# Kernel optimization log

Hardware: AMD Instinct MI355X
Metric: run time of the kernel (lower is better)

## Reference

```python
import jax, jax.numpy as jnp
import numpy as np

B, T, F, U = 256, 512, 128, 1024  # batch, seq_len, feature dim, lstm units


def setup_inputs() -> dict:
    key = jax.random.key(0)
    ks = jax.random.split(key, 11)
    s = jnp.float32(0.05)  # small init so tanh/sigmoid stay in useful range
    f32 = jnp.float32
    return {
        "input_tensor": jax.random.normal(ks[0], (B, T, F), f32),
        # encoder LSTM weights (keras gate order i,f,c,o packed along last axis)
        "enc_Wx": jax.random.normal(ks[1], (F, 4 * U), f32) * s,
        "enc_Wh": jax.random.normal(ks[2], (U, 4 * U), f32) * s,
        "enc_b": jax.random.normal(ks[3], (4 * U,), f32) * s,
        # decoder LSTMCell weights (input dim = U, since it is fed its own output)
        "dec_Wx": jax.random.normal(ks[4], (U, 4 * U), f32) * s,
        "dec_Wh": jax.random.normal(ks[5], (U, 4 * U), f32) * s,
        "dec_b": jax.random.normal(ks[6], (4 * U,), f32) * s,
        # dense1: U -> U with relu; dense2: U -> F linear
        "d1_W": jax.random.normal(ks[7], (U, U), f32) * s,
        "d1_b": jax.random.normal(ks[8], (U,), f32) * s,
        "d2_W": jax.random.normal(ks[9], (U, F), f32) * s,
        "d2_b": jax.random.normal(ks[10], (F,), f32) * s,
    }


def _lstm_step(Wx, Wh, b):
    """Standard keras LSTM cell step. Gate packing order: i, f, g(cand), o."""
    def step(carry, x_t):
        h, c = carry
        z = x_t @ Wx + h @ Wh + b  # [B, 4U]
        i, f, g, o = jnp.split(z, 4, axis=-1)
        c = jax.nn.sigmoid(f) * c + jax.nn.sigmoid(i) * jnp.tanh(g)
        h = jax.nn.sigmoid(o) * jnp.tanh(c)
        return (h, c), h
    return step


def reference(input_tensor, enc_Wx, enc_Wh, enc_b, dec_Wx, dec_Wh, dec_b,
              d1_W, d1_b, d2_W, d2_b):
    x = input_tensor
    b_sz, t_len = x.shape[0], x.shape[1]
    u = enc_Wh.shape[0]
    h0 = jnp.zeros((b_sz, u), x.dtype)

    # Encoder: run LSTM over time, keep only final (h, c) (return_state=True).
    (h, c), _ = jax.lax.scan(_lstm_step(enc_Wx, enc_Wh, enc_b), (h0, h0),
                             jnp.swapaxes(x, 0, 1))  # xs: [T, B, F]

    # Decoder: feed previous output back as input, T steps.
    dec_step = _lstm_step(dec_Wx, dec_Wh, dec_b)
    def dec(carry, _):
        x_in, hh, cc = carry
        (hh, cc), _ = dec_step((hh, cc), x_in)
        return (hh, hh, cc), hh  # next input is the new hidden output

    _, hs = jax.lax.scan(dec, (h, h, c), None, length=t_len)  # hs: [T, B, U]

    # Per-step projections, fused over all timesteps (same math as in-loop dense).
    y = jnp.maximum(hs @ d1_W + d1_b, 0.0) @ d2_W + d2_b  # [T, B, F]
    return jnp.swapaxes(y, 0, 1)  # [B, T, F]
```

## Files before the change

kernel.cpp:

```cpp
#include <hip/hip_runtime.h>
#include <hip/hip_bf16.h>
#include <math.h>
#include <stdio.h>


typedef __attribute__((ext_vector_type(8))) short short8;
typedef __attribute__((ext_vector_type(4))) float f32x4;

#define MFMA(a, b, c) __builtin_amdgcn_mfma_f32_16x16x32_bf16(a, b, c, 0, 0, 0)

__device__ __forceinline__ short f2bf(float f) {
  union { __hip_bfloat16 h; short s; } u;
  u.h = __float2bfloat16(f);
  return u.s;
}
__device__ __forceinline__ void split3(float x, short& a, short& b, short& c) {
  union { __hip_bfloat16 h; short s; } u;
  u.h = __float2bfloat16(x); a = u.s;
  float r1 = x - __bfloat162float(u.h);
  u.h = __float2bfloat16(r1); b = u.s;
  float r2 = r1 - __bfloat162float(u.h);
  u.h = __float2bfloat16(r2); c = u.s;
}
__device__ __forceinline__ float sigm(float x) { return 1.0f / (1.0f + expf(-x)); }

__global__ void pack_w(const float* __restrict__ a, const float* __restrict__ b,
                       short8* __restrict__ dst, int KC, int mode, int ncols,
                       int limbs) {
  int gid = blockIdx.x * 256 + threadIdx.x;
  int lane = gid & 63;
  int kc = (gid >> 6) % KC;
  int nt = gid / (KC * 64);
  int u16 = lane & 15, kq = lane >> 4;
  int kbase = kc * 32 + kq * 8;
  int col;
  if (mode <= 1) { int g = nt & 3, ub = nt >> 2; col = g * 1024 + ub * 16 + u16; }
  else col = nt * 16 + u16;
  short8 v0, v1, v2;
#pragma unroll
  for (int j = 0; j < 8; ++j) {
    int k = kbase + j;
    float x;
    if (mode == 0)      x = a[(size_t)k * 4096 + col] + b[(size_t)k * 4096 + col];
    else if (mode == 1) x = (k < 1024) ? a[(size_t)k * 4096 + col]
                                       : b[(size_t)(k - 1024) * 4096 + col];
    else                x = a[(size_t)k * ncols + col];
    short sa, sb, sc; split3(x, sa, sb, sc);
    v0[j] = sa; v1[j] = sb; v2[j] = sc;
  }
  if (limbs == 3) {
    size_t base = (size_t)(nt * KC + kc) * 3 * 64 + lane;
    dst[base] = v0; dst[base + 64] = v1; dst[base + 128] = v2;
  } else {
    dst[(size_t)(nt * KC + kc) * 64 + lane] = v0;
  }
}

__global__ void pack_x32(const float* __restrict__ src, short8* __restrict__ dst,
                         int t0) {
  int gid = blockIdx.x * 256 + threadIdx.x;
  int lane = gid & 63;
  int kx = (gid >> 6) & 3;
  int mt = (gid >> 8) & 15;
  int tloc = gid >> 12;
  int bb = mt * 16 + (lane & 15);
  int fb = kx * 32 + (lane >> 4) * 8;
  const float* s = src + ((size_t)bb * 512 + (t0 + tloc)) * 128 + fb;
  short8 v0, v1, v2;
#pragma unroll
  for (int j = 0; j < 8; ++j) {
    short sa, sb, sc; split3(s[j], sa, sb, sc);
    v0[j] = sa; v1[j] = sb; v2[j] = sc;
  }
  size_t base = (size_t)((tloc * 16 + mt) * 4 + kx) * 3 * 64 + lane;
  dst[base] = v0; dst[base + 64] = v1; dst[base + 128] = v2;
}

__global__ void zero_f(float* p, int n) {
  int i = blockIdx.x * 256 + threadIdx.x;
  if (i < n) p[i] = 0.f;
}

__global__ __launch_bounds__(512) void lstm_step(
    const short8* __restrict__ Ah, const short8* __restrict__ Ax,
    const short8* __restrict__ W, const float* __restrict__ bias,
    float* __restrict__ cst, short8* __restrict__ Hnext,
    short8* __restrict__ Hring, int KC) {
  int tid = threadIdx.x;
  int lane = tid & 63, wv = tid >> 6;
  int wr = wv & 3, wc = wv >> 2;
  int xcd = blockIdx.x & 7, idx = blockIdx.x >> 3;
  int mb = idx & 3, ub = xcd * 8 + (idx >> 2);
  int mt = mb * 4 + wr;
  int nt0 = ub * 4 + wc * 2, nt1 = nt0 + 1;
  const f32x4 z4 = {0.f, 0.f, 0.f, 0.f};
  f32x4 acc0 = z4, acc1 = z4;
  for (int kc = 0; kc < KC; ++kc) {
    const short8* Ap = (kc < 32)
        ? (Ah + ((size_t)(mt * 32 + kc) * 3) * 64 + lane)
        : (Ax + ((size_t)(mt * 4 + (kc - 32)) * 3) * 64 + lane);
    short8 a0 = Ap[0], a1 = Ap[64], a2 = Ap[128];
    const short8* Bp = W + ((size_t)(nt0 * KC + kc) * 3) * 64 + lane;
    const short8* Bq = W + ((size_t)(nt1 * KC + kc) * 3) * 64 + lane;
    short8 b00 = Bp[0], b01 = Bp[64], b02 = Bp[128];
    short8 b10 = Bq[0], b11 = Bq[64], b12 = Bq[128];
    acc0 = MFMA(a0, b00, acc0);  acc1 = MFMA(a0, b10, acc1);
    acc0 = MFMA(a0, b01, acc0);  acc1 = MFMA(a0, b11, acc1);
    acc0 = MFMA(a1, b00, acc0);  acc1 = MFMA(a1, b10, acc1);
    acc0 = MFMA(a1, b01, acc0);  acc1 = MFMA(a1, b11, acc1);
    acc0 = MFMA(a0, b02, acc0);  acc1 = MFMA(a0, b12, acc1);
    acc0 = MFMA(a2, b00, acc0);  acc1 = MFMA(a2, b10, acc1);
  }

  __shared__ float zt[64][68];
  int u16 = lane & 15, quad = lane >> 4;
  float bv0 = bias[(wc * 2 + 0) * 1024 + ub * 16 + u16];
  float bv1 = bias[(wc * 2 + 1) * 1024 + ub * 16 + u16];
#pragma unroll
  for (int r = 0; r < 4; ++r) {
    zt[wr * 16 + quad * 4 + r][(wc * 2 + 0) * 16 + u16] = acc0[r] + bv0;
    zt[wr * 16 + quad * 4 + r][(wc * 2 + 1) * 16 + u16] = acc1[r] + bv1;
  }
  __syncthreads();

  if (tid < 128) {
    int r = tid >> 1, s = tid & 1;
    int m = mb * 64 + r;
    int ubase = ub * 16 + s * 8;
    float* cp = cst + (size_t)m * 1024 + ubase;
    short8 h0, h1, h2;
#pragma unroll
    for (int j = 0; j < 8; ++j) {
      int uu = s * 8 + j;
      float iv = zt[r][uu];
      float fv = zt[r][16 + uu];
      float gv = zt[r][32 + uu];
      float ov = zt[r][48 + uu];
      float cn = sigm(fv) * cp[j] + sigm(iv) * tanhf(gv);
      cp[j] = cn;
      float hval = sigm(ov) * tanhf(cn);
      short sa, sb, sc; split3(hval, sa, sb, sc);
      h0[j] = sa; h1[j] = sb; h2[j] = sc;
    }
    int mtw = m >> 4, r16 = m & 15;
    int kcw = ubase >> 5, ko = ubase & 31;
    int lane_t = r16 + 16 * (ko >> 3);
    size_t base = ((size_t)(mtw * 32 + kcw) * 3) * 64 + lane_t;
    Hnext[base] = h0; Hnext[base + 64] = h1; Hnext[base + 128] = h2;
    if (Hring)
      Hring[(size_t)(mtw * 32 + kcw) * 64 + lane_t] = h0;
  }
}

__global__ __launch_bounds__(256) void proj(
    const short8* __restrict__ HS, const short8* __restrict__ W1,
    const float* __restrict__ b1, const short8* __restrict__ W2,
    const float* __restrict__ b2, float* __restrict__ out, int t0) {
  int tid = threadIdx.x;
  int lane = tid & 63, wv = tid >> 6;
  int wr = wv & 1, wc = wv >> 1;
  int tloc = blockIdx.x >> 2, mb = blockIdx.x & 3;
  int t = t0 + tloc;
  const short8* A = HS + (size_t)tloc * 16 * 32 * 64;
  int u16 = lane & 15, quad = lane >> 4;
  int mt0 = mb * 4 + wr * 2;
  __shared__ short a1f[4][8][512];
  const f32x4 z4 = {0.f, 0.f, 0.f, 0.f};
  f32x4 acc2[2][4];
#pragma unroll
  for (int i = 0; i < 2; ++i)
#pragma unroll
    for (int jj = 0; jj < 4; ++jj) acc2[i][jj] = z4;

  for (int q = 0; q < 4; ++q) {
    f32x4 acc1[2][8];
#pragma unroll
    for (int i = 0; i < 2; ++i)
#pragma unroll
      for (int n = 0; n < 8; ++n) acc1[i][n] = z4;
    for (int kc = 0; kc < 32; ++kc) {
      short8 av0 = A[(size_t)(mt0 * 32 + kc) * 64 + lane];
      short8 av1 = A[(size_t)((mt0 + 1) * 32 + kc) * 64 + lane];
#pragma unroll
      for (int n = 0; n < 8; ++n) {
        int nt = q * 16 + wc * 8 + n;
        short8 bv = W1[(size_t)(nt * 32 + kc) * 64 + lane];
        acc1[0][n] = MFMA(av0, bv, acc1[0][n]);
        acc1[1][n] = MFMA(av1, bv, acc1[1][n]);
      }
    }
    __syncthreads();
#pragma unroll
    for (int i = 0; i < 2; ++i)
#pragma unroll
      for (int n = 0; n < 8; ++n)
#pragma unroll
        for (int r = 0; r < 4; ++r) {
          int rl = wr * 32 + i * 16 + quad * 4 + r;
          int nloc = wc * 128 + n * 16 + u16;
          float v = fmaxf(acc1[i][n][r] + b1[q * 256 + nloc], 0.f);
          int mtl = rl >> 4, r16 = rl & 15;
          int kcl = nloc >> 5, ko = nloc & 31;
          a1f[mtl][kcl][(r16 + 16 * (ko >> 3)) * 8 + (ko & 7)] = f2bf(v);
        }
    __syncthreads();
    for (int kcl = 0; kcl < 8; ++kcl) {
      short8 av0 = *(const short8*)&a1f[wr * 2 + 0][kcl][lane * 8];
      short8 av1 = *(const short8*)&a1f[wr * 2 + 1][kcl][lane * 8];
#pragma unroll
      for (int jj = 0; jj < 4; ++jj) {
        int nt2 = wc * 4 + jj;
        short8 bv = W2[(size_t)(nt2 * 32 + q * 8 + kcl) * 64 + lane];
        acc2[0][jj] = MFMA(av0, bv, acc2[0][jj]);
        acc2[1][jj] = MFMA(av1, bv, acc2[1][jj]);
      }
    }
  }
#pragma unroll
  for (int i = 0; i < 2; ++i)
#pragma unroll
    for (int jj = 0; jj < 4; ++jj)
#pragma unroll
      for (int r = 0; r < 4; ++r) {
        int rl = wr * 32 + i * 16 + quad * 4 + r;
        int f = wc * 64 + jj * 16 + u16;
        int bb = mb * 64 + rl;
        out[((size_t)bb * 512 + t) * 128 + f] = acc2[i][jj][r] + b2[f];
      }
}

extern "C" void kernel_launch(void* const* d_in, const int* in_sizes, int n_in,
                              void* d_out, int out_size, void* d_ws, size_t ws_size,
                              hipStream_t stream) {
  const float* x     = (const float*)d_in[0];
  const float* encWx = (const float*)d_in[1];
  const float* encWh = (const float*)d_in[2];
  const float* encb  = (const float*)d_in[3];
  const float* decWx = (const float*)d_in[4];
  const float* decWh = (const float*)d_in[5];
  const float* decb  = (const float*)d_in[6];
  const float* d1W   = (const float*)d_in[7];
  const float* d1b   = (const float*)d_in[8];
  const float* d2W   = (const float*)d_in[9];
  const float* d2b   = (const float*)d_in[10];

  char* ws = (char*)d_ws;
  size_t off = 0;
  short8* Wenc = (short8*)(ws + off); off += (size_t)256 * 36 * 3 * 64 * 16;
  short8* Wdec = (short8*)(ws + off); off += (size_t)256 * 32 * 3 * 64 * 16;
  short8* W1   = (short8*)(ws + off); off += (size_t)64 * 32 * 64 * 16;
  short8* W2   = (short8*)(ws + off); off += (size_t)8 * 32 * 64 * 16;
  short8* Xr   = (short8*)(ws + off); off += (size_t)32 * 16 * 4 * 3 * 64 * 16;
  short8* Hb   = (short8*)(ws + off); off += (size_t)2 * 16 * 32 * 3 * 64 * 16;
  short8* Hring= (short8*)(ws + off); off += (size_t)32 * 16 * 32 * 64 * 16;
  float*  cst  = (float*)(ws + off);  off += (size_t)256 * 1024 * 4;
  (void)in_sizes; (void)n_in; (void)out_size;
  if (ws_size < off) {
    fprintf(stderr, "kernel_launch: ws_size=%zu < needed=%zu -- aborting launch\n",
            ws_size, off);
    return;
  }

  pack_w<<<2304, 256, 0, stream>>>(encWh, encWx, Wenc, 36, 1, 4096, 3);
  pack_w<<<2048, 256, 0, stream>>>(decWx, decWh, Wdec, 32, 0, 4096, 3);
  pack_w<<<512, 256, 0, stream>>>(d1W, nullptr, W1, 32, 2, 1024, 1);
  pack_w<<<64, 256, 0, stream>>>(d2W, nullptr, W2, 32, 3, 128, 1);
  zero_f<<<1536, 256, 0, stream>>>((float*)Hb, 16 * 32 * 3 * 64 * 8);
  zero_f<<<1024, 256, 0, stream>>>(cst, 256 * 1024);

  const size_t H3 = (size_t)16 * 32 * 3 * 64;
  const size_t XT = (size_t)16 * 4 * 3 * 64;
  const size_t HR = (size_t)16 * 32 * 64;

  for (int c = 0; c < 16; ++c) {
    pack_x32<<<512, 256, 0, stream>>>(x, Xr, c * 32);
    for (int i = 0; i < 32; ++i) {
      int t = c * 32 + i;
      lstm_step<<<256, 512, 0, stream>>>(Hb + (size_t)(t & 1) * H3, Xr + (size_t)i * XT,
                                         Wenc, encb, cst,
                                         Hb + (size_t)((t + 1) & 1) * H3, nullptr, 36);
    }
  }
  for (int c = 0; c < 16; ++c) {
    for (int i = 0; i < 32; ++i) {
      int d = c * 32 + i;
      lstm_step<<<256, 512, 0, stream>>>(Hb + (size_t)(d & 1) * H3, nullptr,
                                         Wdec, decb, cst,
                                         Hb + (size_t)((d + 1) & 1) * H3,
                                         Hring + (size_t)i * HR, 32);
    }
    proj<<<128, 256, 0, stream>>>(Hring, W1, d1b, W2, d2b, (float*)d_out, c * 32);
  }
}
```

Before: 38.12 ms.

## Fuse 32 LSTM steps per persistent cooperative kernel with per-row-group barriers

Replaces the per-timestep lstm_step launches with a cooperative lstm_seg kernel that runs 32 steps in a loop. Blocks that share a batch row group sync through a global atomic counter/generation barrier instead of a kernel boundary. Blocks are widened to 1024 threads so each wave computes one gate tile instead of two. This removes kernel launch and drain overhead between steps, at the cost of spin-wait barriers and a dependence on all 256 blocks being co-resident.

```diff
diff --git a/kernel.cpp b/kernel.cpp
--- a/kernel.cpp
+++ b/kernel.cpp
@@ -81,74 +81,104 @@
   if (i < n) p[i] = 0.f;
 }
 
-__global__ __launch_bounds__(512) void lstm_step(
-    const short8* __restrict__ Ah, const short8* __restrict__ Ax,
-    const short8* __restrict__ W, const float* __restrict__ bias,
-    float* __restrict__ cst, short8* __restrict__ Hnext,
-    short8* __restrict__ Hring, int KC) {
+__global__ __launch_bounds__(1024) void lstm_seg(
+    const short8* __restrict__ Ax, const short8* __restrict__ W,
+    const float* __restrict__ bias, float* __restrict__ cst,
+    short8* __restrict__ Hb, short8* __restrict__ Hring,
+    int KC, int gstep, int nsteps, unsigned* __restrict__ bar) {
   int tid = threadIdx.x;
   int lane = tid & 63, wv = tid >> 6;
   int wr = wv & 3, wc = wv >> 2;
   int xcd = blockIdx.x & 7, idx = blockIdx.x >> 3;
   int mb = idx & 3, ub = xcd * 8 + (idx >> 2);
   int mt = mb * 4 + wr;
-  int nt0 = ub * 4 + wc * 2, nt1 = nt0 + 1;
-  const f32x4 z4 = {0.f, 0.f, 0.f, 0.f};
-  f32x4 acc0 = z4, acc1 = z4;
-  for (int kc = 0; kc < KC; ++kc) {
-    const short8* Ap = (kc < 32)
-        ? (Ah + ((size_t)(mt * 32 + kc) * 3) * 64 + lane)
-        : (Ax + ((size_t)(mt * 4 + (kc - 32)) * 3) * 64 + lane);
-    short8 a0 = Ap[0], a1 = Ap[64], a2 = Ap[128];
-    const short8* Bp = W + ((size_t)(nt0 * KC + kc) * 3) * 64 + lane;
-    const short8* Bq = W + ((size_t)(nt1 * KC + kc) * 3) * 64 + lane;
-    short8 b00 = Bp[0], b01 = Bp[64], b02 = Bp[128];
-    short8 b10 = Bq[0], b11 = Bq[64], b12 = Bq[128];
-    acc0 = MFMA(a0, b00, acc0);  acc1 = MFMA(a0, b10, acc1);
-    acc0 = MFMA(a0, b01, acc0);  acc1 = MFMA(a0, b11, acc1);
-    acc0 = MFMA(a1, b00, acc0);  acc1 = MFMA(a1, b10, acc1);
-    acc0 = MFMA(a1, b01, acc0);  acc1 = MFMA(a1, b11, acc1);
-    acc0 = MFMA(a0, b02, acc0);  acc1 = MFMA(a0, b12, acc1);
-    acc0 = MFMA(a2, b00, acc0);  acc1 = MFMA(a2, b10, acc1);
-  }
-
+  int nt = ub * 4 + wc;
+  int u16 = lane & 15, quad = lane >> 4;
+  const size_t H3 = (size_t)16 * 32 * 3 * 64;
+  const size_t XT = (size_t)16 * 4 * 3 * 64;
+  const size_t HR = (size_t)16 * 32 * 64;
   __shared__ float zt[64][68];
-  int u16 = lane & 15, quad = lane >> 4;
-  float bv0 = bias[(wc * 2 + 0) * 1024 + ub * 16 + u16];
-  float bv1 = bias[(wc * 2 + 1) * 1024 + ub * 16 + u16];
-#pragma unroll
-  for (int r = 0; r < 4; ++r) {
-    zt[wr * 16 + quad * 4 + r][(wc * 2 + 0) * 16 + u16] = acc0[r] + bv0;
-    zt[wr * 16 + quad * 4 + r][(wc * 2 + 1) * 16 + u16] = acc1[r] + bv1;
-  }
-  __syncthreads();
-
-  if (tid < 128) {
-    int r = tid >> 1, s = tid & 1;
-    int m = mb * 64 + r;
-    int ubase = ub * 16 + s * 8;
-    float* cp = cst + (size_t)m * 1024 + ubase;
-    short8 h0, h1, h2;
-#pragma unroll
-    for (int j = 0; j < 8; ++j) {
-      int uu = s * 8 + j;
-      float iv = zt[r][uu];
-      float fv = zt[r][16 + uu];
-      float gv = zt[r][32 + uu];
-      float ov = zt[r][48 + uu];
-      float cn = sigm(fv) * cp[j] + sigm(iv) * tanhf(gv);
-      cp[j] = cn;
-      float hval = sigm(ov) * tanhf(cn);
-      short sa, sb, sc; split3(hval, sa, sb, sc);
-      h0[j] = sa; h1[j] = sb; h2[j] = sc;
-    }
-    int mtw = m >> 4, r16 = m & 15;
-    int kcw = ubase >> 5, ko = ubase & 31;
-    int lane_t = r16 + 16 * (ko >> 3);
-    size_t base = ((size_t)(mtw * 32 + kcw) * 3) * 64 + lane_t;
-    Hnext[base] = h0; Hnext[base + 64] = h1; Hnext[base + 128] = h2;
-    if (Hring)
-      Hring[(size_t)(mtw * 32 + kcw) * 64 + lane_t] = h0;
+  float bv = bias[wc * 1024 + ub * 16 + u16];
+  unsigned* cnt = bar + mb;
+  unsigned* gen = bar + 4 + mb;
+
+  for (int i = 0; i < nsteps; ++i) {
+    int t = gstep + i;
+    const short8* Ah = Hb + (size_t)(t & 1) * H3;
+    short8* Hnext = Hb + (size_t)((t + 1) & 1) * H3;
+    const short8* Axs = Ax ? (Ax + (size_t)i * XT) : nullptr;
+    const f32x4 z4 = {0.f, 0.f, 0.f, 0.f};
+    f32x4 acc = z4;
+    const short8* Bp = W + ((size_t)nt * KC) * 3 * 64 + lane;
+    for (int kc = 0; kc < KC; ++kc) {
+      const short8* Ap = (kc < 32)
+          ? (Ah + ((size_t)(mt * 32 + kc) * 3) * 64 + lane)
+          : (Axs + ((size_t)(mt * 4 + (kc - 32)) * 3) * 64 + lane);
+      short8 a0 = Ap[0], a1 = Ap[64], a2 = Ap[128];
+      short8 b0 = Bp[0], b1 = Bp[64], b2 = Bp[128];
+      Bp += 192;
+      acc = MFMA(a0, b0, acc);
+      acc = MFMA(a0, b1, acc);
+      acc = MFMA(a1, b0, acc);
+      acc = MFMA(a1, b1, acc);
+      acc = MFMA(a0, b2, acc);
+      acc = MFMA(a2, b0, acc);
+    }
+
+#pragma unroll
+    for (int r = 0; r < 4; ++r)
+      zt[wr * 16 + quad * 4 + r][wc * 16 + u16] = acc[r] + bv;
+    __syncthreads();
+
+    if (tid < 128) {
+      int r = tid >> 1, s = tid & 1;
+      int m = mb * 64 + r;
+      int ubase = ub * 16 + s * 8;
+      float* cp = cst + (size_t)m * 1024 + ubase;
+      short8 h0, h1, h2;
+#pragma unroll
+      for (int j = 0; j < 8; ++j) {
+        int uu = s * 8 + j;
+        float iv = zt[r][uu];
+        float fv = zt[r][16 + uu];
+        float gv = zt[r][32 + uu];
+        float ov = zt[r][48 + uu];
+        float cn = sigm(fv) * cp[j] + sigm(iv) * tanhf(gv);
+        cp[j] = cn;
+        float hval = sigm(ov) * tanhf(cn);
+        short sa, sb, sc; split3(hval, sa, sb, sc);
+        h0[j] = sa; h1[j] = sb; h2[j] = sc;
+      }
+      int mtw = m >> 4, r16 = m & 15;
+      int kcw = ubase >> 5, ko = ubase & 31;
+      int lane_t = r16 + 16 * (ko >> 3);
+      size_t base = ((size_t)(mtw * 32 + kcw) * 3) * 64 + lane_t;
+      Hnext[base] = h0; Hnext[base + 64] = h1; Hnext[base + 128] = h2;
+      if (Hring)
+        Hring[(size_t)i * HR + (size_t)(mtw * 32 + kcw) * 64 + lane_t] = h0;
+    }
+    __syncthreads();
+
+    if (i + 1 < nsteps) {
+      if (tid == 0) {
+        __threadfence();
+        unsigned tick = (unsigned)(t + 1);
+        unsigned old = __hip_atomic_fetch_add(cnt, 1u, __ATOMIC_ACQ_REL,
+                                              __HIP_MEMORY_SCOPE_AGENT);
+        if (old == 63u) {
+          __hip_atomic_store(cnt, 0u, __ATOMIC_RELAXED,
+                             __HIP_MEMORY_SCOPE_AGENT);
+          __hip_atomic_store(gen, tick, __ATOMIC_RELEASE,
+                             __HIP_MEMORY_SCOPE_AGENT);
+        } else {
+          while (__hip_atomic_load(gen, __ATOMIC_RELAXED,
+                                   __HIP_MEMORY_SCOPE_AGENT) < tick)
+            __builtin_amdgcn_s_sleep(1);
+        }
+        __threadfence();
+      }
+      __syncthreads();
+    }
   }
 }
 
@@ -254,6 +284,7 @@
   short8* Hb   = (short8*)(ws + off); off += (size_t)2 * 16 * 32 * 3 * 64 * 16;
   short8* Hring= (short8*)(ws + off); off += (size_t)32 * 16 * 32 * 64 * 16;
   float*  cst  = (float*)(ws + off);  off += (size_t)256 * 1024 * 4;
+  unsigned* bar = (unsigned*)(ws + off); off += 256;
   (void)in_sizes; (void)n_in; (void)out_size;
   if (ws_size < off) {
     fprintf(stderr, "kernel_launch: ws_size=%zu < needed=%zu -- aborting launch\n",
@@ -267,27 +298,31 @@
   pack_w<<<64, 256, 0, stream>>>(d2W, nullptr, W2, 32, 3, 128, 1);
   zero_f<<<1536, 256, 0, stream>>>((float*)Hb, 16 * 32 * 3 * 64 * 8);
   zero_f<<<1024, 256, 0, stream>>>(cst, 256 * 1024);
-
-  const size_t H3 = (size_t)16 * 32 * 3 * 64;
-  const size_t XT = (size_t)16 * 4 * 3 * 64;
-  const size_t HR = (size_t)16 * 32 * 64;
+  zero_f<<<1, 256, 0, stream>>>((float*)bar, 8);
 
   for (int c = 0; c < 16; ++c) {
     pack_x32<<<512, 256, 0, stream>>>(x, Xr, c * 32);
-    for (int i = 0; i < 32; ++i) {
-      int t = c * 32 + i;
-      lstm_step<<<256, 512, 0, stream>>>(Hb + (size_t)(t & 1) * H3, Xr + (size_t)i * XT,
-                                         Wenc, encb, cst,
-                                         Hb + (size_t)((t + 1) & 1) * H3, nullptr, 36);
+    const short8* axp = Xr; const short8* wp = Wenc; const float* bp = encb;
+    float* cp = cst; short8* hbp = Hb; short8* hrp = nullptr;
+    int kcv = 36, gs = c * 32, ns = 32; unsigned* barp = bar;
+    void* args[] = {&axp, &wp, &bp, &cp, &hbp, &hrp, &kcv, &gs, &ns, &barp};
+    hipError_t e = hipLaunchCooperativeKernel((const void*)lstm_seg, dim3(256),
+                                              dim3(1024), args, 0, stream);
+    if (e != hipSuccess) {
+      fprintf(stderr, "coop launch failed (enc c=%d): %s\n", c, hipGetErrorString(e));
+      return;
     }
   }
   for (int c = 0; c < 16; ++c) {
-    for (int i = 0; i < 32; ++i) {
-      int d = c * 32 + i;
-      lstm_step<<<256, 512, 0, stream>>>(Hb + (size_t)(d & 1) * H3, nullptr,
-                                         Wdec, decb, cst,
-                                         Hb + (size_t)((d + 1) & 1) * H3,
-                                         Hring + (size_t)i * HR, 32);
+    const short8* axp = nullptr; const short8* wp = Wdec; const float* bp = decb;
+    float* cp = cst; short8* hbp = Hb; short8* hrp = Hring;
+    int kcv = 32, gs = 512 + c * 32, ns = 32; unsigned* barp = bar;
+    void* args[] = {&axp, &wp, &bp, &cp, &hbp, &hrp, &kcv, &gs, &ns, &barp};
+    hipError_t e = hipLaunchCooperativeKernel((const void*)lstm_seg, dim3(256),
+                                              dim3(1024), args, 0, stream);
+    if (e != hipSuccess) {
+      fprintf(stderr, "coop launch failed (dec c=%d): %s\n", c, hipGetErrorString(e));
+      return;
     }
     proj<<<128, 256, 0, stream>>>(Hring, W1, d1b, W2, d2b, (float*)d_out, c * 32);
   }
```

New measurement: 63.17 ms. +65.7%, slower.
